# Kernel optimization log

Hardware: AMD Instinct MI355X
Metric: run time of the kernel (lower is better)

Reference implementation:

```python
import jax, jax.numpy as jnp
import numpy as np

N = 100000      # nodes
E = 1600000     # edges (avg degree 16)
F_IN = 256      # num_features
H2 = 128        # nhid * 2 (layer 1 width)
H = 64          # nhid (layer 2 width)
C = 10          # num_classes


def setup_inputs() -> dict:
    key = jax.random.key(0)
    ks = jax.random.split(key, 8)
    x = jax.random.normal(ks[0], (N, F_IN), dtype=jnp.float32)
    edge_index = jax.random.randint(ks[1], (2, E), 0, N, dtype=jnp.int64)
    W1 = jax.random.normal(ks[2], (F_IN, H2), dtype=jnp.float32) / np.float32(np.sqrt(F_IN))
    b1 = jnp.zeros((H2,), jnp.float32)
    W2 = jax.random.normal(ks[3], (H2, H), dtype=jnp.float32) / np.float32(np.sqrt(H2))
    b2 = jnp.zeros((H,), jnp.float32)
    Wl = jax.random.normal(ks[4], (H, C), dtype=jnp.float32) / np.float32(np.sqrt(H))
    bl = jnp.zeros((C,), jnp.float32)
    return {"x": x, "edge_index": edge_index, "W1": W1, "b1": b1,
            "W2": W2, "b2": b2, "Wl": Wl, "bl": bl}


def reference(x, edge_index, W1, b1, W2, b2, Wl, bl):
    # --- GCN normalization with self-loops (PyG GCNConv default) ---
    loops = jnp.arange(N, dtype=edge_index.dtype)
    src = jnp.concatenate([edge_index[0], loops])  # message sources
    dst = jnp.concatenate([edge_index[1], loops])  # message targets
    deg = jax.ops.segment_sum(jnp.ones(src.shape[0], x.dtype), dst, num_segments=N)
    dinv = jnp.where(deg > 0, jax.lax.rsqrt(deg), 0.0)
    norm = dinv[src] * dinv[dst]                   # [E+N]

    def gcn_conv(h, W, b):
        m = h @ W                                  # transform first (out_channels small)
        agg = jax.ops.segment_sum(m[src] * norm[:, None], dst, num_segments=N)
        return agg + b

    h = jax.nn.relu(gcn_conv(x, W1, b1))           # [N, H2]
    h = jax.nn.relu(gcn_conv(h, W2, b2))           # [N, H]
    logits = h @ Wl + bl                            # [N, C]
    return jax.nn.log_softmax(logits, axis=-1)
```

## Files before the change

### kernel.cpp

```cpp
#include <hip/hip_runtime.h>


typedef unsigned short ushort_t;
typedef unsigned int uint_t;
typedef __attribute__((ext_vector_type(8))) short short8;
typedef __attribute__((ext_vector_type(4))) float floatx4;

static __device__ __forceinline__ ushort_t f2bf(float f) {
    union { float f; uint_t u; } c; c.f = f;
    return (ushort_t)((c.u + 0x8000u) >> 16);
}
static __device__ __forceinline__ float bf2f(ushort_t h) {
    union { uint_t u; float f; } c; c.u = ((uint_t)h) << 16;
    return c.f;
}
static __device__ __forceinline__ float2 up2(uint_t p) {
    union { uint_t u; float f; } lo, hi;
    lo.u = p << 16; hi.u = p & 0xffff0000u;
    return make_float2(lo.f, hi.f);
}
static __device__ __forceinline__ void ld_lds16(void* lds, const void* g) {
    __builtin_amdgcn_global_load_lds(
        (const __attribute__((address_space(1))) unsigned int*)g,
        (__attribute__((address_space(3))) unsigned int*)lds, 16, 0, 0);
}


__global__ __launch_bounds__(256) void deg_pos_kernel(
    const int* __restrict__ dst, int* __restrict__ cnt8, int* __restrict__ pos,
    int E, int N) {
    int* cnt = cnt8 + (size_t)(blockIdx.x & 7) * N;
    int i8 = (blockIdx.x * 256 + threadIdx.x) * 8;
    if (i8 + 7 < E) {
        int4 d0 = *(const int4*)(dst + i8);
        int4 d1 = *(const int4*)(dst + i8 + 4);
        int4 p0, p1;
        p0.x = atomicAdd(&cnt[d0.x], 1);
        p0.y = atomicAdd(&cnt[d0.y], 1);
        p0.z = atomicAdd(&cnt[d0.z], 1);
        p0.w = atomicAdd(&cnt[d0.w], 1);
        p1.x = atomicAdd(&cnt[d1.x], 1);
        p1.y = atomicAdd(&cnt[d1.y], 1);
        p1.z = atomicAdd(&cnt[d1.z], 1);
        p1.w = atomicAdd(&cnt[d1.w], 1);
        *(int4*)(pos + i8) = p0;
        *(int4*)(pos + i8 + 4) = p1;
    } else {
        for (int e = i8; e < E; e++)
            pos[e] = atomicAdd(&cnt[dst[e]], 1);
    }
}

__global__ void scan_block(const int* __restrict__ cnt8, int* __restrict__ rowptr,
                           int* __restrict__ bsums, float* __restrict__ dinv,
                           int n, int N) {
    __shared__ int s[256];
    int i = blockIdx.x * 256 + threadIdx.x;
    int v = 0;
    if (i < n) {
        #pragma unroll
        for (int c = 0; c < 8; c++) v += cnt8[(size_t)c * N + i];
        dinv[i] = rsqrtf((float)(v + 1));
    }
    s[threadIdx.x] = v;
    __syncthreads();
    for (int off = 1; off < 256; off <<= 1) {
        int t = (threadIdx.x >= off) ? s[threadIdx.x - off] : 0;
        __syncthreads();
        s[threadIdx.x] += t;
        __syncthreads();
    }
    if (i < n) rowptr[i] = s[threadIdx.x] - v;
    if (threadIdx.x == 255) bsums[blockIdx.x] = s[255];
}

__global__ void scan_tops(const int* __restrict__ bsums, int* __restrict__ boffs, int nb) {
    __shared__ int s[512];
    int v = (threadIdx.x < nb) ? bsums[threadIdx.x] : 0;
    s[threadIdx.x] = v;
    __syncthreads();
    for (int off = 1; off < 512; off <<= 1) {
        int t = (threadIdx.x >= off) ? s[threadIdx.x - off] : 0;
        __syncthreads();
        s[threadIdx.x] += t;
        __syncthreads();
    }
    if (threadIdx.x < nb) boffs[threadIdx.x] = s[threadIdx.x] - v;
}

__global__ void finalize_rowptr(int* __restrict__ rowptr, const int* __restrict__ boffs,
                                int n, int E) {
    int i = blockIdx.x * 256 + threadIdx.x;
    if (i < n) rowptr[i] += boffs[blockIdx.x];
    if (i == 0) rowptr[n] = E;
}

__global__ void base_kernel(const int* __restrict__ cnt8, const int* __restrict__ rowptr,
                            int* __restrict__ base8, int n, int N) {
    int i = blockIdx.x * 256 + threadIdx.x;
    if (i < n) {
        int b = rowptr[i];
        #pragma unroll
        for (int c = 0; c < 8; c++) {
            base8[(size_t)c * N + i] = b;
            b += cnt8[(size_t)c * N + i];
        }
    }
}

__global__ __launch_bounds__(256) void place_kernel(
    const int* __restrict__ src, const int* __restrict__ dst,
    const int* __restrict__ pos, const int* __restrict__ base8,
    int* __restrict__ csr, int E, int N) {
    const int* base = base8 + (size_t)(blockIdx.x & 7) * N;
    int i8 = (blockIdx.x * 256 + threadIdx.x) * 8;
    if (i8 + 7 < E) {
        int4 s0 = *(const int4*)(src + i8);
        int4 s1 = *(const int4*)(src + i8 + 4);
        int4 d0 = *(const int4*)(dst + i8);
        int4 d1 = *(const int4*)(dst + i8 + 4);
        int4 p0 = *(const int4*)(pos + i8);
        int4 p1 = *(const int4*)(pos + i8 + 4);
        csr[base[d0.x] + p0.x] = s0.x;
        csr[base[d0.y] + p0.y] = s0.y;
        csr[base[d0.z] + p0.z] = s0.z;
        csr[base[d0.w] + p0.w] = s0.w;
        csr[base[d1.x] + p1.x] = s1.x;
        csr[base[d1.y] + p1.y] = s1.y;
        csr[base[d1.z] + p1.z] = s1.z;
        csr[base[d1.w] + p1.w] = s1.w;
    } else {
        for (int e = i8; e < E; e++)
            csr[base[dst[e]] + pos[e]] = src[e];
    }
}

__global__ void wcvt2_kernel(const float* __restrict__ W1, const float* __restrict__ W2,
                             ushort_t* __restrict__ W1t, ushort_t* __restrict__ W2t) {
    int i = blockIdx.x * 256 + threadIdx.x;
    if (i < 256 * 128) {
        int k = i / 128, n = i % 128;
        W1t[n * 256 + k] = f2bf(W1[i]);
    }
    int j = i - 256 * 128;
    if (j >= 0 && j < 128 * 64) {
        int k = j / 64, n = j % 64;
        W2t[n * 128 + k] = f2bf(W2[j]);
    }
}

__global__ __launch_bounds__(256) void gemm1_mfma(
    const float* __restrict__ A, const ushort_t* __restrict__ Bt,
    const float* __restrict__ dinv, ushort_t* __restrict__ out, int M) {
    __shared__ float    As[2][128 * 32];
    __shared__ ushort_t Bs[2][128 * 32];
    const int tid = threadIdx.x;
    const int l = tid & 63;
    const int wave = tid >> 6;
    const int wm = wave >> 1, wn = wave & 1;
    const int lrow = l & 15, hh = l >> 4;
    const int m0 = blockIdx.x * 128;

    int aslot0[4], aslot1[4], bslot[4];
    #pragma unroll
    for (int mt = 0; mt < 4; mt++) {
        int r = wm * 64 + mt * 16 + lrow;
        int sw = r & 7;
        aslot0[mt] = (r * 8 + ((2 * hh) ^ sw)) * 4;
        aslot1[mt] = (r * 8 + ((2 * hh + 1) ^ sw)) * 4;
    }
    #pragma unroll
    for (int nt = 0; nt < 4; nt++) {
        int nc = wn * 64 + nt * 16 + lrow;
        bslot[nt] = (nc * 4 + (hh ^ ((nc >> 2) & 3))) * 8;
    }

    floatx4 acc[4][4];
    #pragma unroll
    for (int mt = 0; mt < 4; mt++)
        #pragma unroll
        for (int nt = 0; nt < 4; nt++)
            acc[mt][nt] = (floatx4){0.f, 0.f, 0.f, 0.f};

    auto stage = [&](int buf, int k0) {
        #pragma unroll
        for (int i = 0; i < 4; i++) {
            int s = i * 256 + tid;
            int r = s >> 3, cp = s & 7;
            int cg = cp ^ (r & 7);
            int row = m0 + r; if (row >= M) row = M - 1;
            ld_lds16(&As[buf][s * 4], A + (size_t)row * 256 + k0 + cg * 4);
        }
        #pragma unroll
        for (int i = 0; i < 2; i++) {
            int s = i * 256 + tid;
            int nn = s >> 2, cp = s & 3;
            int cg = cp ^ ((nn >> 2) & 3);
            ld_lds16(&Bs[buf][s * 8], Bt + (size_t)nn * 256 + k0 + cg * 8);
        }
    };

    stage(0, 0);
    __syncthreads();
    int buf = 0;
    for (int kk = 0; kk < 8; kk++) {
        if (kk < 7) stage(buf ^ 1, (kk + 1) * 32);
        short8 afr[4], bfr[4];
        #pragma unroll
        for (int mt = 0; mt < 4; mt++) {
            float4 u = *(const float4*)&As[buf][aslot0[mt]];
            float4 v = *(const float4*)&As[buf][aslot1[mt]];
            short8 t;
            t[0] = (short)f2bf(u.x); t[1] = (short)f2bf(u.y);
            t[2] = (short)f2bf(u.z); t[3] = (short)f2bf(u.w);
            t[4] = (short)f2bf(v.x); t[5] = (short)f2bf(v.y);
            t[6] = (short)f2bf(v.z); t[7] = (short)f2bf(v.w);
            afr[mt] = t;
        }
        #pragma unroll
        for (int nt = 0; nt < 4; nt++)
            bfr[nt] = *(const short8*)&Bs[buf][bslot[nt]];
        #pragma unroll
        for (int mt = 0; mt < 4; mt++)
            #pragma unroll
            for (int nt = 0; nt < 4; nt++)
                acc[mt][nt] = __builtin_amdgcn_mfma_f32_16x16x32_bf16(
                    afr[mt], bfr[nt], acc[mt][nt], 0, 0, 0);
        __syncthreads();
        buf ^= 1;
    }

    const int r0 = hh * 4;
    #pragma unroll
    for (int mt = 0; mt < 4; mt++) {
        int mbase = m0 + wm * 64 + mt * 16 + r0;
        float4 dv = *(const float4*)&dinv[mbase];
        float d[4] = {dv.x, dv.y, dv.z, dv.w};
        #pragma unroll
        for (int i = 0; i < 4; i++) {
            int m = mbase + i;
            if (m < M) {
                #pragma unroll
                for (int nt = 0; nt < 4; nt++)
                    out[(size_t)m * 128 + wn * 64 + nt * 16 + lrow] =
                        f2bf(acc[mt][nt][i] * d[i]);
            }
        }
    }
}

__global__ __launch_bounds__(256) void gemm2_mfma(
    const ushort_t* __restrict__ A, const ushort_t* __restrict__ Bt,
    const float* __restrict__ dinv, ushort_t* __restrict__ out, int M) {
    __shared__ ushort_t As[2][128 * 32];
    __shared__ ushort_t Bs[2][64 * 32];
    const int tid = threadIdx.x;
    const int l = tid & 63;
    const int wave = tid >> 6;
    const int wm = wave >> 1, wn = wave & 1;
    const int lrow = l & 15, hh = l >> 4;
    const int m0 = blockIdx.x * 128;

    int aslot[4], bslot[2];
    #pragma unroll
    for (int mt = 0; mt < 4; mt++) {
        int r = wm * 64 + mt * 16 + lrow;
        aslot[mt] = (r * 4 + (hh ^ ((r >> 2) & 3))) * 8;
    }
    #pragma unroll
    for (int nt = 0; nt < 2; nt++) {
        int nc = wn * 32 + nt * 16 + lrow;
        bslot[nt] = (nc * 4 + (hh ^ ((nc >> 2) & 3))) * 8;
    }

    floatx4 acc[4][2];
    #pragma unroll
    for (int mt = 0; mt < 4; mt++)
        #pragma unroll
        for (int nt = 0; nt < 2; nt++)
            acc[mt][nt] = (floatx4){0.f, 0.f, 0.f, 0.f};

    auto stage = [&](int buf, int k0) {
        #pragma unroll
        for (int i = 0; i < 2; i++) {
            int s = i * 256 + tid;
            int r = s >> 2, cp = s & 3;
            int cg = cp ^ ((r >> 2) & 3);
            int row = m0 + r; if (row >= M) row = M - 1;
            ld_lds16(&As[buf][s * 8], A + (size_t)row * 128 + k0 + cg * 8);
        }
        {
            int s = tid;
            int nn = s >> 2, cp = s & 3;
            int cg = cp ^ ((nn >> 2) & 3);
            ld_lds16(&Bs[buf][s * 8], Bt + (size_t)nn * 128 + k0 + cg * 8);
        }
    };

    stage(0, 0);
    __syncthreads();
    int buf = 0;
    for (int kk = 0; kk < 4; kk++) {
        if (kk < 3) stage(buf ^ 1, (kk + 1) * 32);
        short8 afr[4], bfr[2];
        #pragma unroll
        for (int mt = 0; mt < 4; mt++)
            afr[mt] = *(const short8*)&As[buf][aslot[mt]];
        #pragma unroll
        for (int nt = 0; nt < 2; nt++)
            bfr[nt] = *(const short8*)&Bs[buf][bslot[nt]];
        #pragma unroll
        for (int mt = 0; mt < 4; mt++)
            #pragma unroll
            for (int nt = 0; nt < 2; nt++)
                acc[mt][nt] = __builtin_amdgcn_mfma_f32_16x16x32_bf16(
                    afr[mt], bfr[nt], acc[mt][nt], 0, 0, 0);
        __syncthreads();
        buf ^= 1;
    }

    const int r0 = hh * 4;
    #pragma unroll
    for (int mt = 0; mt < 4; mt++) {
        int mbase = m0 + wm * 64 + mt * 16 + r0;
        float4 dv = *(const float4*)&dinv[mbase];
        float d[4] = {dv.x, dv.y, dv.z, dv.w};
        #pragma unroll
        for (int i = 0; i < 4; i++) {
            int m = mbase + i;
            if (m < M) {
                #pragma unroll
                for (int nt = 0; nt < 2; nt++)
                    out[(size_t)m * 64 + wn * 32 + nt * 16 + lrow] =
                        f2bf(acc[mt][nt][i] * d[i]);
            }
        }
    }
}

__global__ __launch_bounds__(256) void spmm_relu128(
    const ushort_t* __restrict__ Mm, const int* __restrict__ rowptr,
    const int* __restrict__ csr, const float* __restrict__ dinv,
    const float* __restrict__ bias, ushort_t* __restrict__ out, int n) {
    int v = (blockIdx.x * 256 + threadIdx.x) >> 6;
    int lane = threadIdx.x & 63;
    if (v >= n) return;
    int jb = rowptr[v], je = rowptr[v + 1];
    int cntn = je - jb;
    const char* Mb = (const char*)Mm;
    const uint_t loff = lane * 4;

    float2 accA = up2(*(const uint_t*)(Mb + ((size_t)v << 8) + loff));
    float2 accB = make_float2(0.f, 0.f);

    for (int base = 0; base < cntn; base += 64) {
        int m = cntn - base; if (m > 64) m = 64;
        int roff = (base + lane < cntn) ? (csr[jb + base + lane] << 8) : 0;
        int jj = 0;
        for (; jj + 16 <= m; jj += 16) {
            uint_t o[16];
            #pragma unroll
            for (int t = 0; t < 16; t++) o[t] = (uint_t)__shfl(roff, jj + t) + loff;
            uint_t p[16];
            #pragma unroll
            for (int t = 0; t < 16; t++) p[t] = *(const uint_t*)(Mb + o[t]);
            #pragma unroll
            for (int t = 0; t < 16; t++) {
                float2 f = up2(p[t]);
                if (t & 1) { accB.x += f.x; accB.y += f.y; }
                else       { accA.x += f.x; accA.y += f.y; }
            }
        }
        for (; jj + 8 <= m; jj += 8) {
            uint_t o[8];
            #pragma unroll
            for (int t = 0; t < 8; t++) o[t] = (uint_t)__shfl(roff, jj + t) + loff;
            uint_t p[8];
            #pragma unroll
            for (int t = 0; t < 8; t++) p[t] = *(const uint_t*)(Mb + o[t]);
            #pragma unroll
            for (int t = 0; t < 8; t++) {
                float2 f = up2(p[t]);
                if (t & 1) { accB.x += f.x; accB.y += f.y; }
                else       { accA.x += f.x; accA.y += f.y; }
            }
        }
        for (; jj < m; jj++) {
            uint_t o = (uint_t)__shfl(roff, jj) + loff;
            float2 f = up2(*(const uint_t*)(Mb + o));
            accA.x += f.x; accA.y += f.y;
        }
    }
    float d = dinv[v];
    float2 bv = *(const float2*)&bias[lane * 2];
    float rx = fmaxf(d * (accA.x + accB.x) + bv.x, 0.f);
    float ry = fmaxf(d * (accA.y + accB.y) + bv.y, 0.f);
    uint_t packed = ((uint_t)f2bf(ry) << 16) | (uint_t)f2bf(rx);
    *(uint_t*)(out + (size_t)v * 128 + lane * 2) = packed;
}

__global__ __launch_bounds__(256) void spmm_relu64(
    const ushort_t* __restrict__ Mm, const int* __restrict__ rowptr,
    const int* __restrict__ csr, const float* __restrict__ dinv,
    const float* __restrict__ bias, ushort_t* __restrict__ out, int n) {
    int v = (blockIdx.x * 256 + threadIdx.x) >> 6;
    int lane = threadIdx.x & 63;
    if (v >= n) return;
    int jb = rowptr[v], je = rowptr[v + 1];
    int cntn = je - jb;
    const char* Mb = (const char*)Mm;
    const uint_t loff = lane * 2;

    float accA = bf2f(*(const ushort_t*)(Mb + ((size_t)v << 7) + loff));
    float accB = 0.f;

    for (int base = 0; base < cntn; base += 64) {
        int m = cntn - base; if (m > 64) m = 64;
        int roff = (base + lane < cntn) ? (csr[jb + base + lane] << 7) : 0;
        int jj = 0;
        for (; jj + 16 <= m; jj += 16) {
            uint_t o[16];
            #pragma unroll
            for (int t = 0; t < 16; t++) o[t] = (uint_t)__shfl(roff, jj + t) + loff;
            ushort_t p[16];
            #pragma unroll
            for (int t = 0; t < 16; t++) p[t] = *(const ushort_t*)(Mb + o[t]);
            #pragma unroll
            for (int t = 0; t < 16; t++) {
                if (t & 1) accB += bf2f(p[t]);
                else       accA += bf2f(p[t]);
            }
        }
        for (; jj + 8 <= m; jj += 8) {
            uint_t o[8];
            #pragma unroll
            for (int t = 0; t < 8; t++) o[t] = (uint_t)__shfl(roff, jj + t) + loff;
            ushort_t p[8];
            #pragma unroll
            for (int t = 0; t < 8; t++) p[t] = *(const ushort_t*)(Mb + o[t]);
            #pragma unroll
            for (int t = 0; t < 8; t++) {
                if (t & 1) accB += bf2f(p[t]);
                else       accA += bf2f(p[t]);
            }
        }
        for (; jj < m; jj++) {
            uint_t o = (uint_t)__shfl(roff, jj) + loff;
            accA += bf2f(*(const ushort_t*)(Mb + o));
        }
    }
    float r = fmaxf(dinv[v] * (accA + accB) + bias[lane], 0.f);
    out[(size_t)v * 64 + lane] = f2bf(r);
}

__global__ __launch_bounds__(256) void head_kernel(
    const ushort_t* __restrict__ h2, const float* __restrict__ Wl,
    const float* __restrict__ bl, float* __restrict__ out, int n) {
    __shared__ float Ws[64 * 10];
    __shared__ float bs[10];
    for (int i = threadIdx.x; i < 640; i += 256) Ws[i] = Wl[i];
    if (threadIdx.x < 10) bs[threadIdx.x] = bl[threadIdx.x];
    __syncthreads();
    int v = blockIdx.x * 256 + threadIdx.x;
    if (v >= n) return;
    float acc[10];
    #pragma unroll
    for (int c = 0; c < 10; c++) acc[c] = bs[c];
    const ushort_t* hrow = &h2[(size_t)v * 64];
    #pragma unroll
    for (int k0 = 0; k0 < 64; k0 += 8) {
        short8 hv = *(const short8*)&hrow[k0];
        #pragma unroll
        for (int kk = 0; kk < 8; kk++) {
            float hf = bf2f((ushort_t)hv[kk]);
            #pragma unroll
            for (int c = 0; c < 10; c++)
                acc[c] += hf * Ws[(k0 + kk) * 10 + c];
        }
    }
    float m = acc[0];
    #pragma unroll
    for (int c = 1; c < 10; c++) m = fmaxf(m, acc[c]);
    float s = 0.f;
    #pragma unroll
    for (int c = 0; c < 10; c++) s += expf(acc[c] - m);
    float lse = logf(s);
    #pragma unroll
    for (int c = 0; c < 10; c++) out[(size_t)v * 10 + c] = acc[c] - m - lse;
}

extern "C" void kernel_launch(void* const* d_in, const int* in_sizes, int n_in,
                              void* d_out, int out_size, void* d_ws, size_t ws_size,
                              hipStream_t stream) {
    const float* x   = (const float*)d_in[0];
    const int*   ei  = (const int*)d_in[1];
    const float* W1  = (const float*)d_in[2];
    const float* b1  = (const float*)d_in[3];
    const float* W2  = (const float*)d_in[4];
    const float* b2  = (const float*)d_in[5];
    const float* Wl  = (const float*)d_in[6];
    const float* bl  = (const float*)d_in[7];
    float*       out = (float*)d_out;

    const int N = in_sizes[0] / 256;
    const int E = in_sizes[1] / 2;
    const int* srcI = ei;
    const int* dstI = ei + E;

    char* ws = (char*)d_ws;
    size_t off = 0;
    auto alloc = [&](size_t bytes) -> void* {
        void* p = ws + off;
        off = (off + bytes + 255) & ~(size_t)255;
        return p;
    };
    int*      cnt8   = (int*)alloc((size_t)N * 8 * 4);
    int*      base8  = (int*)alloc((size_t)N * 8 * 4);
    int*      rowptr = (int*)alloc((size_t)(N + 1) * 4);
    float*    dinv   = (float*)alloc((size_t)(N + 128) * 4);
    int*      csr    = (int*)alloc((size_t)E * 4);
    int*      pos    = (int*)alloc((size_t)E * 4);
    int*      bsums  = (int*)alloc(512 * 4);
    int*      boffs  = (int*)alloc(512 * 4);
    ushort_t* W1t    = (ushort_t*)alloc((size_t)128 * 256 * 2);
    ushort_t* W2t    = (ushort_t*)alloc((size_t)64 * 128 * 2);
    ushort_t* bufA   = (ushort_t*)alloc((size_t)N * 128 * 2);
    ushort_t* bufB   = (ushort_t*)alloc((size_t)N * 128 * 2);

    hipMemsetAsync(cnt8, 0, (size_t)N * 8 * 4, stream);

    const int nb = (N + 255) / 256;
    const int eb8 = (E + 2047) / 2048;
    deg_pos_kernel<<<eb8, 256, 0, stream>>>(dstI, cnt8, pos, E, N);
    scan_block<<<nb, 256, 0, stream>>>(cnt8, rowptr, bsums, dinv, N, N);
    scan_tops<<<1, 512, 0, stream>>>(bsums, boffs, nb);
    finalize_rowptr<<<nb, 256, 0, stream>>>(rowptr, boffs, N, E);
    base_kernel<<<nb, 256, 0, stream>>>(cnt8, rowptr, base8, N, N);
    place_kernel<<<eb8, 256, 0, stream>>>(srcI, dstI, pos, base8, csr, E, N);

    wcvt2_kernel<<<(256 * 128 + 128 * 64 + 255) / 256, 256, 0, stream>>>(W1, W2, W1t, W2t);

    const int gblk = (N + 127) / 128;
    gemm1_mfma<<<gblk, 256, 0, stream>>>(x, W1t, dinv, bufA, N);
    spmm_relu128<<<(N + 3) / 4, 256, 0, stream>>>(bufA, rowptr, csr, dinv, b1, bufB, N);
    gemm2_mfma<<<gblk, 256, 0, stream>>>(bufB, W2t, dinv, bufA, N);
    spmm_relu64<<<(N + 3) / 4, 256, 0, stream>>>(bufA, rowptr, csr, dinv, b2, bufB, N);
    head_kernel<<<(N + 255) / 256, 256, 0, stream>>>(bufB, Wl, bl, out, N);
}
```

Measured before the change: 430.2 us.

## Build CSR via two-level bucket sort with LDS histograms instead of global atomics

Replaces the global-atomic degree count, multi-pass scan and placement kernels with a bucketed counting sort. Each block histograms destinations into 128-node buckets in LDS, buckets are scanned per block, and edges are scattered into bucket-contiguous packed records (src plus local dst bits). A per-bucket kernel then sorts its edges in LDS to produce rowptr, csr and dinv. The aim is to remove contended global atomics, the memset, and several launches. In exchange it caps a bucket at 4096 edges, so a skewed degree distribution would silently truncate. Packing src into 17 bits limits N to 131072.

```diff
diff --git a/kernel.cpp b/kernel.cpp
--- a/kernel.cpp
+++ b/kernel.cpp
@@ -25,113 +25,159 @@
         (__attribute__((address_space(3))) unsigned int*)lds, 16, 0, 0);
 }
 
-
-__global__ __launch_bounds__(256) void deg_pos_kernel(
-    const int* __restrict__ dst, int* __restrict__ cnt8, int* __restrict__ pos,
-    int E, int N) {
-    int* cnt = cnt8 + (size_t)(blockIdx.x & 7) * N;
+#define NBMAX 800
+#define ECAP  4096
+
+__global__ __launch_bounds__(256) void hist_kernel(
+    const int* __restrict__ dst, int* __restrict__ histG, int E, int NB) {
+    __shared__ int h[NBMAX];
+    for (int i = threadIdx.x; i < NB; i += 256) h[i] = 0;
+    __syncthreads();
     int i8 = (blockIdx.x * 256 + threadIdx.x) * 8;
     if (i8 + 7 < E) {
         int4 d0 = *(const int4*)(dst + i8);
         int4 d1 = *(const int4*)(dst + i8 + 4);
-        int4 p0, p1;
-        p0.x = atomicAdd(&cnt[d0.x], 1);
-        p0.y = atomicAdd(&cnt[d0.y], 1);
-        p0.z = atomicAdd(&cnt[d0.z], 1);
-        p0.w = atomicAdd(&cnt[d0.w], 1);
-        p1.x = atomicAdd(&cnt[d1.x], 1);
-        p1.y = atomicAdd(&cnt[d1.y], 1);
-        p1.z = atomicAdd(&cnt[d1.z], 1);
-        p1.w = atomicAdd(&cnt[d1.w], 1);
-        *(int4*)(pos + i8) = p0;
-        *(int4*)(pos + i8 + 4) = p1;
+        atomicAdd(&h[d0.x >> 7], 1);
+        atomicAdd(&h[d0.y >> 7], 1);
+        atomicAdd(&h[d0.z >> 7], 1);
+        atomicAdd(&h[d0.w >> 7], 1);
+        atomicAdd(&h[d1.x >> 7], 1);
+        atomicAdd(&h[d1.y >> 7], 1);
+        atomicAdd(&h[d1.z >> 7], 1);
+        atomicAdd(&h[d1.w >> 7], 1);
     } else {
-        for (int e = i8; e < E; e++)
-            pos[e] = atomicAdd(&cnt[dst[e]], 1);
-    }
-}
-
-__global__ void scan_block(const int* __restrict__ cnt8, int* __restrict__ rowptr,
-                           int* __restrict__ bsums, float* __restrict__ dinv,
-                           int n, int N) {
+        for (int e = i8; e < E; e++) atomicAdd(&h[dst[e] >> 7], 1);
+    }
+    __syncthreads();
+    int* out = histG + (size_t)blockIdx.x * NB;
+    for (int i = threadIdx.x; i < NB; i += 256) out[i] = h[i];
+}
+
+__global__ __launch_bounds__(256) void scan_bucket(
+    int* __restrict__ histG, int* __restrict__ totG, int GB, int NB) {
     __shared__ int s[256];
-    int i = blockIdx.x * 256 + threadIdx.x;
-    int v = 0;
-    if (i < n) {
-        #pragma unroll
-        for (int c = 0; c < 8; c++) v += cnt8[(size_t)c * N + i];
-        dinv[i] = rsqrtf((float)(v + 1));
-    }
-    s[threadIdx.x] = v;
-    __syncthreads();
-    for (int off = 1; off < 256; off <<= 1) {
-        int t = (threadIdx.x >= off) ? s[threadIdx.x - off] : 0;
-        __syncthreads();
-        s[threadIdx.x] += t;
-        __syncthreads();
-    }
-    if (i < n) rowptr[i] = s[threadIdx.x] - v;
-    if (threadIdx.x == 255) bsums[blockIdx.x] = s[255];
-}
-
-__global__ void scan_tops(const int* __restrict__ bsums, int* __restrict__ boffs, int nb) {
-    __shared__ int s[512];
-    int v = (threadIdx.x < nb) ? bsums[threadIdx.x] : 0;
-    s[threadIdx.x] = v;
-    __syncthreads();
-    for (int off = 1; off < 512; off <<= 1) {
-        int t = (threadIdx.x >= off) ? s[threadIdx.x - off] : 0;
-        __syncthreads();
-        s[threadIdx.x] += t;
-        __syncthreads();
-    }
-    if (threadIdx.x < nb) boffs[threadIdx.x] = s[threadIdx.x] - v;
-}
-
-__global__ void finalize_rowptr(int* __restrict__ rowptr, const int* __restrict__ boffs,
-                                int n, int E) {
-    int i = blockIdx.x * 256 + threadIdx.x;
-    if (i < n) rowptr[i] += boffs[blockIdx.x];
-    if (i == 0) rowptr[n] = E;
-}
-
-__global__ void base_kernel(const int* __restrict__ cnt8, const int* __restrict__ rowptr,
-                            int* __restrict__ base8, int n, int N) {
-    int i = blockIdx.x * 256 + threadIdx.x;
-    if (i < n) {
-        int b = rowptr[i];
-        #pragma unroll
-        for (int c = 0; c < 8; c++) {
-            base8[(size_t)c * N + i] = b;
-            b += cnt8[(size_t)c * N + i];
-        }
-    }
-}
-
-__global__ __launch_bounds__(256) void place_kernel(
+    const int b = blockIdx.x;
+    const int t = threadIdx.x;
+    int running = 0;
+    int nch = (GB + 255) / 256;
+    for (int c = 0; c < nch; c++) {
+        int j = c * 256 + t;
+        int v = (j < GB) ? histG[(size_t)j * NB + b] : 0;
+        s[t] = v;
+        __syncthreads();
+        for (int off = 1; off < 256; off <<= 1) {
+            int tmp = (t >= off) ? s[t - off] : 0;
+            __syncthreads();
+            s[t] += tmp;
+            __syncthreads();
+        }
+        if (j < GB) histG[(size_t)j * NB + b] = s[t] - v + running;
+        int ctot = s[255];
+        __syncthreads();
+        running += ctot;
+    }
+    if (t == 0) totG[b] = running;
+}
+
+__global__ void scan_tot(const int* __restrict__ totG, int* __restrict__ bbase,
+                         int NB) {
+    __shared__ int s[256];
+    const int t = threadIdx.x;
+    int running = 0;
+    int nch = (NB + 255) / 256;
+    for (int c = 0; c < nch; c++) {
+        int j = c * 256 + t;
+        int v = (j < NB) ? totG[j] : 0;
+        s[t] = v;
+        __syncthreads();
+        for (int off = 1; off < 256; off <<= 1) {
+            int tmp = (t >= off) ? s[t - off] : 0;
+            __syncthreads();
+            s[t] += tmp;
+            __syncthreads();
+        }
+        if (j < NB) bbase[j] = s[t] - v + running;
+        int ctot = s[255];
+        __syncthreads();
+        running += ctot;
+    }
+    if (t == 0) bbase[NB] = running;
+}
+
+__global__ __launch_bounds__(256) void scatter_kernel(
     const int* __restrict__ src, const int* __restrict__ dst,
-    const int* __restrict__ pos, const int* __restrict__ base8,
-    int* __restrict__ csr, int E, int N) {
-    const int* base = base8 + (size_t)(blockIdx.x & 7) * N;
+    const int* __restrict__ histG, const int* __restrict__ bbase,
+    int* __restrict__ packed, int E, int NB) {
+    __shared__ int lbase[NBMAX];
+    const int* row = histG + (size_t)blockIdx.x * NB;
+    for (int i = threadIdx.x; i < NB; i += 256)
+        lbase[i] = bbase[i] + row[i];
+    __syncthreads();
     int i8 = (blockIdx.x * 256 + threadIdx.x) * 8;
     if (i8 + 7 < E) {
         int4 s0 = *(const int4*)(src + i8);
         int4 s1 = *(const int4*)(src + i8 + 4);
         int4 d0 = *(const int4*)(dst + i8);
         int4 d1 = *(const int4*)(dst + i8 + 4);
-        int4 p0 = *(const int4*)(pos + i8);
-        int4 p1 = *(const int4*)(pos + i8 + 4);
-        csr[base[d0.x] + p0.x] = s0.x;
-        csr[base[d0.y] + p0.y] = s0.y;
-        csr[base[d0.z] + p0.z] = s0.z;
-        csr[base[d0.w] + p0.w] = s0.w;
-        csr[base[d1.x] + p1.x] = s1.x;
-        csr[base[d1.y] + p1.y] = s1.y;
-        csr[base[d1.z] + p1.z] = s1.z;
-        csr[base[d1.w] + p1.w] = s1.w;
+        int p;
+        p = atomicAdd(&lbase[d0.x >> 7], 1); packed[p] = s0.x | ((d0.x & 127) << 17);
+        p = atomicAdd(&lbase[d0.y >> 7], 1); packed[p] = s0.y | ((d0.y & 127) << 17);
+        p = atomicAdd(&lbase[d0.z >> 7], 1); packed[p] = s0.z | ((d0.z & 127) << 17);
+        p = atomicAdd(&lbase[d0.w >> 7], 1); packed[p] = s0.w | ((d0.w & 127) << 17);
+        p = atomicAdd(&lbase[d1.x >> 7], 1); packed[p] = s1.x | ((d1.x & 127) << 17);
+        p = atomicAdd(&lbase[d1.y >> 7], 1); packed[p] = s1.y | ((d1.y & 127) << 17);
+        p = atomicAdd(&lbase[d1.z >> 7], 1); packed[p] = s1.z | ((d1.z & 127) << 17);
+        p = atomicAdd(&lbase[d1.w >> 7], 1); packed[p] = s1.w | ((d1.w & 127) << 17);
     } else {
-        for (int e = i8; e < E; e++)
-            csr[base[dst[e]] + pos[e]] = src[e];
+        for (int e = i8; e < E; e++) {
+            int d = dst[e];
+            int p = atomicAdd(&lbase[d >> 7], 1);
+            packed[p] = src[e] | ((d & 127) << 17);
+        }
+    }
+}
+
+__global__ __launch_bounds__(256) void bucket_csr(
+    const int* __restrict__ packed, const int* __restrict__ bbase,
+    int* __restrict__ rowptr, int* __restrict__ csr,
+    float* __restrict__ dinv, int N, int NB) {
+    __shared__ int ebuf[ECAP];
+    __shared__ int cnt[128];
+    __shared__ int pl[128];
+    __shared__ int s[256];
+    const int b = blockIdx.x;
+    const int t = threadIdx.x;
+    const int lo = bbase[b];
+    const int hi = bbase[b + 1];
+    int m = hi - lo;
+    if (m > ECAP) m = ECAP;
+    for (int i = t; i < m; i += 256) ebuf[i] = packed[lo + i];
+    if (t < 128) cnt[t] = 0;
+    __syncthreads();
+    for (int i = t; i < m; i += 256) atomicAdd(&cnt[ebuf[i] >> 17], 1);
+    __syncthreads();
+    const int node0 = b << 7;
+    int c = (t < 128) ? cnt[t] : 0;
+    if (t < 128 && node0 + t < N)
+        dinv[node0 + t] = rsqrtf((float)(c + 1));
+    s[t] = c;
+    __syncthreads();
+    for (int off = 1; off < 256; off <<= 1) {
+        int tmp = (t >= off) ? s[t - off] : 0;
+        __syncthreads();
+        s[t] += tmp;
+        __syncthreads();
+    }
+    int excl = s[t] - c;
+    if (t < 128) {
+        pl[t] = excl;
+        if (node0 + t <= N) rowptr[node0 + t] = lo + excl;
+    }
+    __syncthreads();
+    for (int i = t; i < m; i += 256) {
+        int e = ebuf[i];
+        int p = atomicAdd(&pl[e >> 17], 1);
+        csr[lo + p] = e & 0x1FFFF;
     }
 }
 
@@ -507,6 +553,9 @@
     const int* srcI = ei;
     const int* dstI = ei + E;
 
+    const int NB = (N + 127) >> 7;
+    const int GB = (E + 2047) / 2048;
+
     char* ws = (char*)d_ws;
     size_t off = 0;
     auto alloc = [&](size_t bytes) -> void* {
@@ -514,29 +563,23 @@
         off = (off + bytes + 255) & ~(size_t)255;
         return p;
     };
-    int*      cnt8   = (int*)alloc((size_t)N * 8 * 4);
-    int*      base8  = (int*)alloc((size_t)N * 8 * 4);
+    int*      histG  = (int*)alloc((size_t)GB * NB * 4);
+    int*      totG   = (int*)alloc((size_t)NB * 4);
+    int*      bbase  = (int*)alloc((size_t)(NB + 1) * 4);
+    int*      packed = (int*)alloc((size_t)E * 4);
     int*      rowptr = (int*)alloc((size_t)(N + 1) * 4);
     float*    dinv   = (float*)alloc((size_t)(N + 128) * 4);
     int*      csr    = (int*)alloc((size_t)E * 4);
-    int*      pos    = (int*)alloc((size_t)E * 4);
-    int*      bsums  = (int*)alloc(512 * 4);
-    int*      boffs  = (int*)alloc(512 * 4);
     ushort_t* W1t    = (ushort_t*)alloc((size_t)128 * 256 * 2);
     ushort_t* W2t    = (ushort_t*)alloc((size_t)64 * 128 * 2);
     ushort_t* bufA   = (ushort_t*)alloc((size_t)N * 128 * 2);
     ushort_t* bufB   = (ushort_t*)alloc((size_t)N * 128 * 2);
 
-    hipMemsetAsync(cnt8, 0, (size_t)N * 8 * 4, stream);
-
-    const int nb = (N + 255) / 256;
-    const int eb8 = (E + 2047) / 2048;
-    deg_pos_kernel<<<eb8, 256, 0, stream>>>(dstI, cnt8, pos, E, N);
-    scan_block<<<nb, 256, 0, stream>>>(cnt8, rowptr, bsums, dinv, N, N);
-    scan_tops<<<1, 512, 0, stream>>>(bsums, boffs, nb);
-    finalize_rowptr<<<nb, 256, 0, stream>>>(rowptr, boffs, N, E);
-    base_kernel<<<nb, 256, 0, stream>>>(cnt8, rowptr, base8, N, N);
-    place_kernel<<<eb8, 256, 0, stream>>>(srcI, dstI, pos, base8, csr, E, N);
+    hist_kernel<<<GB, 256, 0, stream>>>(dstI, histG, E, NB);
+    scan_bucket<<<NB, 256, 0, stream>>>(histG, totG, GB, NB);
+    scan_tot<<<1, 256, 0, stream>>>(totG, bbase, NB);
+    scatter_kernel<<<GB, 256, 0, stream>>>(srcI, dstI, histG, bbase, packed, E, NB);
+    bucket_csr<<<NB, 256, 0, stream>>>(packed, bbase, rowptr, csr, dinv, N, NB);
 
     wcvt2_kernel<<<(256 * 128 + 128 * 64 + 255) / 256, 256, 0, stream>>>(W1, W2, W1t, W2t);
 
```

Result: faster. 371.4 us (-13.7%).
